# Kernel tuning notes

Measured on AMD Instinct MI355X. Metric: run time of the kernel, lower is better.

## Reference

```python
import jax, jax.numpy as jnp
import numpy as np

HIDDEN = 768
HEADS = 12
HEAD_DIM = HIDDEN // HEADS  # 64


def setup_inputs() -> dict:
    key = jax.random.key(0)
    k1, k2, k3 = jax.random.split(key, 3)
    B, N, C = 64, 197, HIDDEN
    hidden_states = jax.random.normal(k1, (B, N, C), dtype=jnp.float32)
    # qkv Linear: weight [C, 3C] (stored transposed for x @ W), bias [3C]
    w_qkv = jax.random.normal(k2, (C, 3 * C), dtype=jnp.float32) * (1.0 / np.sqrt(C))
    b_qkv = jax.random.normal(k3, (3 * C,), dtype=jnp.float32) * 0.02
    return {"hidden_states": hidden_states, "w_qkv": w_qkv, "b_qkv": b_qkv}


def reference(hidden_states, w_qkv, b_qkv):
    B, N, C = hidden_states.shape
    scale = HEAD_DIM ** -0.5
    qkv = hidden_states @ w_qkv + b_qkv                      # [B, N, 3C]
    qkv = qkv.reshape(B, N, 3, HEADS, HEAD_DIM)
    qkv = jnp.transpose(qkv, (2, 0, 3, 1, 4))                # [3, B, H, N, d]
    q, k, v = qkv[0], qkv[1], qkv[2]
    scores = jnp.einsum("bhqd,bhkd->bhqk", q, k) * scale     # [B, H, N, N]
    probs = jax.nn.softmax(scores, axis=-1)
    # dropout is identity in eval mode (p=0.0)
    ctx = jnp.einsum("bhqk,bhkd->bhqd", probs, v)            # [B, H, N, d]
    ctx = jnp.transpose(ctx, (0, 2, 1, 3)).reshape(B, N, C)  # [B, N, C]
    return ctx
```

## Files before the change

### kernel.cpp

```cpp
#include <hip/hip_runtime.h>

#define M_ROWS 12608
#define K_DIM  768
#define XC_ELEMS (64*24*16*512)
#define WC_ELEMS (12*24*12*512)

typedef __bf16 bf16x8 __attribute__((ext_vector_type(8)));
typedef float  f32x4  __attribute__((ext_vector_type(4)));

__device__ __forceinline__ unsigned short f2bf(float f) {
    unsigned u = __builtin_bit_cast(unsigned, f);
    u += 0x7fffu + ((u >> 16) & 1u);
    return (unsigned short)(u >> 16);
}

__device__ __forceinline__ void gll16(const unsigned short* g, unsigned short* l) {
    __builtin_amdgcn_global_load_lds(
        (const __attribute__((address_space(1))) unsigned int*)g,
        (__attribute__((address_space(3))) unsigned int*)l, 16, 0, 0);
}

__global__ __launch_bounds__(256) void prep_kernel(
        const float* __restrict__ X, unsigned short* __restrict__ Xc,
        const float* __restrict__ W, unsigned short* __restrict__ Wc) {
    __shared__ float tile[32][33];
    const int bid = blockIdx.x;
    const int t = threadIdx.x;
    if (bid < 6144) {
        const int cg = bid * 4 + (t >> 6);
        const int lane = t & 63;
        const int p = cg / 384, rem = cg - p * 384;
        const int kt = rem >> 4, c = rem & 15;
        const int kc = c >> 2, rg = c & 3;
        const int grow = p * 197 + rg * 64 + lane;
        uint4 u = (uint4){0, 0, 0, 0};
        if (grow < M_ROWS) {
            const float* src = X + (size_t)grow * K_DIM + kt * 32 + kc * 8;
            float4 a = *(const float4*)src;
            float4 b = *(const float4*)(src + 4);
            u.x = f2bf(a.x) | ((unsigned)f2bf(a.y) << 16);
            u.y = f2bf(a.z) | ((unsigned)f2bf(a.w) << 16);
            u.z = f2bf(b.x) | ((unsigned)f2bf(b.y) << 16);
            u.w = f2bf(b.z) | ((unsigned)f2bf(b.w) << 16);
        }
        *(uint4*)(Xc + (size_t)cg * 512 + lane * 8) = u;
        return;
    }
    const int b2 = bid - 6144;
    const int n0 = (b2 % 72) * 32, k0 = (b2 / 72) * 32;
    const int tx = t & 31, ty = t >> 5;
#pragma unroll
    for (int i = 0; i < 4; ++i)
        tile[ty + i * 8][tx] = W[(size_t)(k0 + ty + i * 8) * 2304 + n0 + tx];
    __syncthreads();
    if (t < 128) {
        const int kc = t >> 5, tx2 = t & 31;
        const int grp = n0 / 768, remn = n0 - grp * 768;
        const int h = remn >> 6, lh = remn & 63;
        const int kt = k0 >> 5;
        uint4 u;
        u.x = f2bf(tile[kc * 8 + 0][tx2]) | ((unsigned)f2bf(tile[kc * 8 + 1][tx2]) << 16);
        u.y = f2bf(tile[kc * 8 + 2][tx2]) | ((unsigned)f2bf(tile[kc * 8 + 3][tx2]) << 16);
        u.z = f2bf(tile[kc * 8 + 4][tx2]) | ((unsigned)f2bf(tile[kc * 8 + 5][tx2]) << 16);
        u.w = f2bf(tile[kc * 8 + 6][tx2]) | ((unsigned)f2bf(tile[kc * 8 + 7][tx2]) << 16);
        *(uint4*)(Wc + (size_t)(((h * 24 + kt) * 12) + kc * 3 + grp) * 512 + (lh + tx2) * 8) = u;
    }
}

__global__ __launch_bounds__(768) void fused_kernel(
        const unsigned short* __restrict__ Xc, const unsigned short* __restrict__ Wc,
        const float* __restrict__ bias, float* __restrict__ out) {
    __shared__ __align__(16) unsigned short L[68304];

    const int t = threadIdx.x;
    const int w = t >> 6, lane = t & 63, quad = lane >> 4, l16 = lane & 15;
    const int wr = w >> 2, wn = w & 3;
    const int wm = w / 3, wnn = w - wm * 3;
    const int wrow0 = wm * 64;
    const int wcol0 = wnn * 64;
    (void)wr; (void)wn;

    const int lin = blockIdx.x;
    const int wg = (lin & 7) * 96 + (lin >> 3);
    const int bb = wg / 12, h = wg - bb * 12;

    const unsigned short* sgp[3];
    int sof[3], gst[3], bst[3];
    const int nst = (w < 4) ? 3 : 2;
    {
        const int clist[3] = {w, w + 12, 24 + w};
#pragma unroll
        for (int s = 0; s < 3; ++s) {
            const int c = clist[s];
            if (c < 16) {
                sgp[s] = Xc + ((size_t)bb * 384 + c) * 512 + lane * 8;
                sof[s] = c * 512; gst[s] = 8192; bst[s] = 8192;
            } else {
                const int cb = c - 16;
                sgp[s] = Wc + ((size_t)h * 288 + cb) * 512 + lane * 8;
                sof[s] = 16384 + cb * 512; gst[s] = 6144; bst[s] = 6144;
            }
        }
    }

    f32x4 acc[4][4];
#pragma unroll
    for (int i = 0; i < 4; ++i)
#pragma unroll
        for (int j = 0; j < 4; ++j) acc[i][j] = (f32x4){0.f, 0.f, 0.f, 0.f};

#pragma unroll
    for (int s = 0; s < 3; ++s)
        if (s < nst) gll16(sgp[s], &L[sof[s]]);
    asm volatile("s_waitcnt vmcnt(0)" ::: "memory");
    __builtin_amdgcn_s_barrier();
    asm volatile("" ::: "memory");

#pragma unroll 2
    for (int kt = 0; kt < 24; ++kt) {
        const int cur = kt & 1, nxt = cur ^ 1;
        const int skt = (kt + 1 < 24 ? kt + 1 : 0);

#pragma unroll
        for (int s = 0; s < 3; ++s)
            if (s < nst) gll16(sgp[s] + (size_t)skt * gst[s], &L[sof[s] + nxt * bst[s]]);

        const unsigned short* Ab = &L[cur * 8192];
        const unsigned short* Bb = &L[16384 + cur * 6144];
        bf16x8 af[4], bq[4];
#pragma unroll
        for (int i = 0; i < 4; ++i)
            af[i] = *(const bf16x8*)&Ab[quad * 2048 + (wrow0 + i * 16 + l16) * 8];
#pragma unroll
        for (int j = 0; j < 4; ++j)
            bq[j] = *(const bf16x8*)&Bb[quad * 1536 + (wcol0 + j * 16 + l16) * 8];

#pragma unroll
        for (int i = 0; i < 4; ++i)
#pragma unroll
            for (int j = 0; j < 4; ++j)
                acc[i][j] = __builtin_amdgcn_mfma_f32_16x16x32_bf16(af[i], bq[j], acc[i][j], 0, 0, 0);

        asm volatile("s_waitcnt vmcnt(0)" ::: "memory");
        __builtin_amdgcn_s_barrier();
        asm volatile("" ::: "memory");
    }

    unsigned short* Qs = &L[0];
    unsigned short* Ks = &L[14184];
    unsigned short* Vt = &L[28368];
    unsigned short* Ps = &L[42192];

    {
        const float bscale = (wnn == 0) ? 0.125f : 1.0f;
#pragma unroll
        for (int j = 0; j < 4; ++j) {
            const int d = j * 16 + l16;
            const float bv = bias[wnn * 768 + h * 64 + d];
#pragma unroll
            for (int i = 0; i < 4; ++i) {
                const int rowb = wrow0 + i * 16 + quad * 4;
#pragma unroll
                for (int r = 0; r < 4; ++r) {
                    const int row = rowb + r;
                    if (row >= 197) continue;
                    const float val = (acc[i][j][r] + bv) * bscale;
                    if (wnn == 0)      Qs[row * 72 + d] = f2bf(val);
                    else if (wnn == 1) Ks[row * 72 + d] = f2bf(val);
                    else               Vt[d * 216 + row] = f2bf(val);
                }
            }
        }
    }
    for (int idx = t; idx < 64 * 19; idx += 768) {
        int d = idx / 19, c = 197 + idx - d * 19;
        Vt[d * 216 + c] = 0;
    }
    __syncthreads();

    unsigned short* Pw = Ps + w * (16 * 136);

    for (int tile = w; tile < 13; tile += 12) {
        int rq = tile * 16 + l16;
        int tokq = rq < 197 ? rq : 196;
        bf16x8 aq0 = *(const bf16x8*)&Qs[tokq * 72 + quad * 8];
        bf16x8 aq1 = *(const bf16x8*)&Qs[tokq * 72 + 32 + quad * 8];

        f32x4 s[13];
        __builtin_amdgcn_s_setprio(1);
#pragma unroll
        for (int c = 0; c < 13; ++c) {
            int krow = c * 16 + l16;
            if (krow > 196) krow = 196;
            bf16x8 kb0 = *(const bf16x8*)&Ks[krow * 72 + quad * 8];
            bf16x8 kb1 = *(const bf16x8*)&Ks[krow * 72 + 32 + quad * 8];
            f32x4 zz = (f32x4){0.f, 0.f, 0.f, 0.f};
            zz = __builtin_amdgcn_mfma_f32_16x16x32_bf16(aq0, kb0, zz, 0, 0, 0);
            zz = __builtin_amdgcn_mfma_f32_16x16x32_bf16(aq1, kb1, zz, 0, 0, 0);
            s[c] = zz;
        }
        __builtin_amdgcn_s_setprio(0);
        if (l16 >= 5) { s[12][0] = -1e30f; s[12][1] = -1e30f; s[12][2] = -1e30f; s[12][3] = -1e30f; }

        float mx[4], lsum[4];
#pragma unroll
        for (int r = 0; r < 4; ++r) {
            float m = s[0][r];
#pragma unroll
            for (int c = 1; c < 13; ++c) m = fmaxf(m, s[c][r]);
#pragma unroll
            for (int d = 1; d < 16; d <<= 1) m = fmaxf(m, __shfl_xor(m, d));
            mx[r] = m;
            lsum[r] = 0.f;
        }
#pragma unroll
        for (int c = 0; c < 13; ++c)
#pragma unroll
            for (int r = 0; r < 4; ++r) {
                float p = __expf(s[c][r] - mx[r]);
                s[c][r] = p;
                lsum[r] += p;
            }
#pragma unroll
        for (int r = 0; r < 4; ++r)
#pragma unroll
            for (int d = 1; d < 16; d <<= 1) lsum[r] += __shfl_xor(lsum[r], d);

        f32x4 o[4];
#pragma unroll
        for (int j = 0; j < 4; ++j) o[j] = (f32x4){0.f, 0.f, 0.f, 0.f};

#pragma unroll
        for (int c = 0; c < 8; ++c)
#pragma unroll
            for (int r = 0; r < 4; ++r)
                Pw[(quad * 4 + r) * 136 + c * 16 + l16] = f2bf(s[c][r]);
        __builtin_amdgcn_s_setprio(1);
#pragma unroll
        for (int kc = 0; kc < 4; ++kc) {
            int kof = kc * 32 + quad * 8;
            bf16x8 ap = *(const bf16x8*)&Pw[l16 * 136 + kof];
#pragma unroll
            for (int j = 0; j < 4; ++j) {
                bf16x8 bv = *(const bf16x8*)&Vt[(j * 16 + l16) * 216 + kof];
                o[j] = __builtin_amdgcn_mfma_f32_16x16x32_bf16(ap, bv, o[j], 0, 0, 0);
            }
        }
        __builtin_amdgcn_s_setprio(0);
#pragma unroll
        for (int r = 0; r < 4; ++r)
            Pw[(quad * 4 + r) * 136 + 80 + l16] = 0;
#pragma unroll
        for (int c = 8; c < 13; ++c)
#pragma unroll
            for (int r = 0; r < 4; ++r)
                Pw[(quad * 4 + r) * 136 + (c - 8) * 16 + l16] = f2bf(s[c][r]);
        __builtin_amdgcn_s_setprio(1);
#pragma unroll
        for (int kc = 0; kc < 3; ++kc) {
            int kofA = kc * 32 + quad * 8;
            int kofB = (kc == 2 && quad >= 2) ? 0 : kofA;
            bf16x8 ap = *(const bf16x8*)&Pw[l16 * 136 + kofA];
#pragma unroll
            for (int j = 0; j < 4; ++j) {
                bf16x8 bv = *(const bf16x8*)&Vt[(j * 16 + l16) * 216 + 128 + kofB];
                o[j] = __builtin_amdgcn_mfma_f32_16x16x32_bf16(ap, bv, o[j], 0, 0, 0);
            }
        }
        __builtin_amdgcn_s_setprio(0);

        int tokbase = tile * 16 + quad * 4;
#pragma unroll
        for (int r = 0; r < 4; ++r) {
            int tr = tokbase + r;
            if (tr >= 197) continue;
            float inv = 1.f / lsum[r];
#pragma unroll
            for (int j = 0; j < 4; ++j)
                out[((size_t)(bb * 197 + tr)) * 768 + h * 64 + j * 16 + l16] = o[j][r] * inv;
        }
    }
}

extern "C" void kernel_launch(void* const* d_in, const int* in_sizes, int n_in,
                              void* d_out, int out_size, void* d_ws, size_t ws_size,
                              hipStream_t stream) {
    const float* X    = (const float*)d_in[0];
    const float* W    = (const float*)d_in[1];
    const float* bias = (const float*)d_in[2];
    float* out = (float*)d_out;

    unsigned short* Xc = (unsigned short*)d_ws;
    unsigned short* Wc = (unsigned short*)d_ws + XC_ELEMS;

    prep_kernel<<<7872, 256, 0, stream>>>(X, Xc, W, Wc);
    fused_kernel<<<768, 768, 0, stream>>>(Xc, Wc, bias, out);
}
```

Before: 203.0 us.

## Load GEMM fragments directly from global into registers, dropping LDS staging

The QKV projection main loop no longer stages X and W tiles into shared memory with global_load_lds and per-iteration barriers. Each wave now reads its MFMA fragments straight from global memory, using register double-buffering across two k-steps per iteration. This removes LDS traffic and block-wide barriers from the GEMM loop. In exchange, tiles that several waves share are fetched redundantly from global/L2, and register pressure rises.

```diff
diff --git a/kernel.cpp b/kernel.cpp
--- a/kernel.cpp
+++ b/kernel.cpp
@@ -12,12 +12,6 @@
     unsigned u = __builtin_bit_cast(unsigned, f);
     u += 0x7fffu + ((u >> 16) & 1u);
     return (unsigned short)(u >> 16);
-}
-
-__device__ __forceinline__ void gll16(const unsigned short* g, unsigned short* l) {
-    __builtin_amdgcn_global_load_lds(
-        (const __attribute__((address_space(1))) unsigned int*)g,
-        (__attribute__((address_space(3))) unsigned int*)l, 16, 0, 0);
 }
 
 __global__ __launch_bounds__(256) void prep_kernel(
@@ -74,34 +68,25 @@
 
     const int t = threadIdx.x;
     const int w = t >> 6, lane = t & 63, quad = lane >> 4, l16 = lane & 15;
-    const int wr = w >> 2, wn = w & 3;
     const int wm = w / 3, wnn = w - wm * 3;
     const int wrow0 = wm * 64;
     const int wcol0 = wnn * 64;
-    (void)wr; (void)wn;
 
     const int lin = blockIdx.x;
     const int wg = (lin & 7) * 96 + (lin >> 3);
     const int bb = wg / 12, h = wg - bb * 12;
 
-    const unsigned short* sgp[3];
-    int sof[3], gst[3], bst[3];
-    const int nst = (w < 4) ? 3 : 2;
-    {
-        const int clist[3] = {w, w + 12, 24 + w};
-#pragma unroll
-        for (int s = 0; s < 3; ++s) {
-            const int c = clist[s];
-            if (c < 16) {
-                sgp[s] = Xc + ((size_t)bb * 384 + c) * 512 + lane * 8;
-                sof[s] = c * 512; gst[s] = 8192; bst[s] = 8192;
-            } else {
-                const int cb = c - 16;
-                sgp[s] = Wc + ((size_t)h * 288 + cb) * 512 + lane * 8;
-                sof[s] = 16384 + cb * 512; gst[s] = 6144; bst[s] = 6144;
-            }
-        }
-    }
+    const unsigned short* pa = Xc + ((size_t)bb * 384 + quad * 4 + wm) * 512 + l16 * 8;
+    const unsigned short* pb = Wc + ((size_t)h * 288 + quad * 3 + wnn) * 512 + l16 * 8;
+
+#define LDA4(d, p) { d[0] = *(const bf16x8*)(p);        d[1] = *(const bf16x8*)((p) + 128); \
+                     d[2] = *(const bf16x8*)((p) + 256); d[3] = *(const bf16x8*)((p) + 384); }
+#define MFMA16(A, B)                                                                  \
+    _Pragma("unroll")                                                                 \
+    for (int i = 0; i < 4; ++i)                                                       \
+        _Pragma("unroll")                                                             \
+        for (int j = 0; j < 4; ++j)                                                   \
+            acc[i][j] = __builtin_amdgcn_mfma_f32_16x16x32_bf16(A[i], B[j], acc[i][j], 0, 0, 0);
 
     f32x4 acc[4][4];
 #pragma unroll
@@ -109,42 +94,18 @@
 #pragma unroll
         for (int j = 0; j < 4; ++j) acc[i][j] = (f32x4){0.f, 0.f, 0.f, 0.f};
 
-#pragma unroll
-    for (int s = 0; s < 3; ++s)
-        if (s < nst) gll16(sgp[s], &L[sof[s]]);
-    asm volatile("s_waitcnt vmcnt(0)" ::: "memory");
-    __builtin_amdgcn_s_barrier();
-    asm volatile("" ::: "memory");
-
-#pragma unroll 2
-    for (int kt = 0; kt < 24; ++kt) {
-        const int cur = kt & 1, nxt = cur ^ 1;
-        const int skt = (kt + 1 < 24 ? kt + 1 : 0);
-
-#pragma unroll
-        for (int s = 0; s < 3; ++s)
-            if (s < nst) gll16(sgp[s] + (size_t)skt * gst[s], &L[sof[s] + nxt * bst[s]]);
-
-        const unsigned short* Ab = &L[cur * 8192];
-        const unsigned short* Bb = &L[16384 + cur * 6144];
-        bf16x8 af[4], bq[4];
-#pragma unroll
-        for (int i = 0; i < 4; ++i)
-            af[i] = *(const bf16x8*)&Ab[quad * 2048 + (wrow0 + i * 16 + l16) * 8];
-#pragma unroll
-        for (int j = 0; j < 4; ++j)
-            bq[j] = *(const bf16x8*)&Bb[quad * 1536 + (wcol0 + j * 16 + l16) * 8];
-
-#pragma unroll
-        for (int i = 0; i < 4; ++i)
-#pragma unroll
-            for (int j = 0; j < 4; ++j)
-                acc[i][j] = __builtin_amdgcn_mfma_f32_16x16x32_bf16(af[i], bq[j], acc[i][j], 0, 0, 0);
-
-        asm volatile("s_waitcnt vmcnt(0)" ::: "memory");
-        __builtin_amdgcn_s_barrier();
-        asm volatile("" ::: "memory");
-    }
+    bf16x8 a0[4], b0[4], a1[4], b1[4];
+    LDA4(a0, pa) LDA4(b0, pb)
+#pragma unroll 3
+    for (int s2 = 0; s2 < 12; ++s2) {
+        LDA4(a1, pa + 8192) LDA4(b1, pb + 6144)
+        MFMA16(a0, b0)
+        pa += 16384; pb += 12288;
+        if (s2 < 11) { LDA4(a0, pa) LDA4(b0, pb) }
+        MFMA16(a1, b1)
+    }
+#undef LDA4
+#undef MFMA16
 
     unsigned short* Qs = &L[0];
     unsigned short* Ks = &L[14184];
```

Result: slower. 211.7 us (+4.3%).
